# Kernel tuning notes

Hardware: AMD Instinct MI355X
Metric: run time of the kernel (lower is better)

## Reference

```python
import jax, jax.numpy as jnp
import numpy as np

D = 128   # opt.geometric_latent_dim
H = 132   # FCBlock hidden width (hardcoded in source)
B = 65536
K = 8

def setup_inputs() -> dict:
    key = jax.random.key(0)
    ks = jax.random.split(key, 16)
    s = lambda k, shp, fan: jax.random.normal(k, shp, jnp.float32) / np.sqrt(fan)
    return {
        "signal": jax.random.normal(ks[0], (B, D), jnp.float32),
        "components": jax.random.normal(ks[1], (K, B, D), jnp.float32),
        # message_map / update_map: Linear(D, D)
        "Wm": s(ks[2], (D, D), D), "bm": jnp.zeros((D,), jnp.float32),
        "Wu": s(ks[3], (D, D), D), "bu": jnp.zeros((D,), jnp.float32),
        "W0": s(ks[4], (H, 2 * D), 2 * D), "b0": jnp.zeros((H,), jnp.float32),
        "W1": s(ks[5], (H, H), H),         "b1": jnp.zeros((H,), jnp.float32),
        "W2": s(ks[6], (H, H), H),         "b2": jnp.zeros((H,), jnp.float32),
        "W3": s(ks[7], (D, H), H),         "b3": jnp.zeros((D,), jnp.float32),
    }

def reference(signal, components, Wm, bm, Wu, bu, W0, b0, W1, b1, W2, b2, W3, b3):
    # message_map applied to each component, then summed over components
    msgs = jnp.einsum('kbd,ed->kbe', components, Wm) + bm  # [K,B,D]
    right = msgs.sum(axis=0)                               # [B,D]
    # update_map
    right = right @ Wu.T + bu                              # [B,D]
    # joint_update: FCBlock on concat([signal, right])
    x = jnp.concatenate([signal, right], axis=-1)          # [B,2D]
    x = jax.nn.relu(x @ W0.T + b0)
    x = jax.nn.relu(x @ W1.T + b1)
    x = jax.nn.relu(x @ W2.T + b2)
    return x @ W3.T + b3                                   # [B,D]
```

## Files before the change

kernel.cpp:

```cpp
#include <hip/hip_runtime.h>
#include <stdint.h>

#define DD  128
#define HH  132
#define BB  65536
#define KKC 8
#define HP  144
#define KP  160

typedef short bf16x8 __attribute__((ext_vector_type(8)));
typedef float f32x4  __attribute__((ext_vector_type(4)));

__device__ __forceinline__ unsigned short f2b(float f){
  union{float f; unsigned u;} c; c.f = f;
  unsigned r = c.u + 0x7fffu + ((c.u >> 16) & 1u);
  return (unsigned short)(r >> 16);
}

__global__ void prepA(const float* __restrict__ Wm, const float* __restrict__ bm,
                      const float* __restrict__ Wu, const float* __restrict__ bu,
                      float* __restrict__ Wf, float* __restrict__ bfv){
  int idx = blockIdx.x * 256 + threadIdx.x;
  int i = idx >> 7, j = idx & 127;
  float acc = 0.f;
  for(int d = 0; d < DD; ++d)
    acc += Wu[i*DD + d] * Wm[d*DD + j];
  Wf[idx] = acc;
  if(j == 0){
    float a = 0.f;
    for(int d = 0; d < DD; ++d) a += Wu[i*DD + d] * bm[d];
    bfv[i] = (float)KKC * a + bu[i];
  }
}

__global__ void prepB(const float* __restrict__ W0, const float* __restrict__ b0,
                      const float* __restrict__ W1, const float* __restrict__ b1,
                      const float* __restrict__ W2, const float* __restrict__ b2,
                      const float* __restrict__ W3, const float* __restrict__ b3,
                      const float* __restrict__ Wf, const float* __restrict__ bfv,
                      unsigned short* __restrict__ w0s_p, unsigned short* __restrict__ w0rp,
                      unsigned short* __restrict__ w1p,  unsigned short* __restrict__ w2p,
                      unsigned short* __restrict__ w3p,
                      float* __restrict__ b0p, float* __restrict__ b1p,
                      float* __restrict__ b2p, float* __restrict__ b3p){
  int idx = blockIdx.x * 256 + threadIdx.x;
  if(idx < HP*DD){
    int n = idx >> 7, k = idx & 127;
    w0s_p[idx] = (n < HH) ? f2b(W0[n*(2*DD) + k]) : (unsigned short)0;
    return;
  }
  idx -= HP*DD;
  if(idx < HP*DD){
    int n = idx >> 7, k = idx & 127;
    float acc = 0.f;
    if(n < HH)
      for(int i = 0; i < DD; ++i)
        acc += W0[n*(2*DD) + DD + i] * Wf[i*DD + k];
    w0rp[idx] = (n < HH) ? f2b(acc) : (unsigned short)0;
    return;
  }
  idx -= HP*DD;
  if(idx < HP*KP){
    int n = idx / KP, k = idx % KP;
    w1p[idx] = (n < HH && k < HH) ? f2b(W1[n*HH + k]) : (unsigned short)0;
    return;
  }
  idx -= HP*KP;
  if(idx < HP*KP){
    int n = idx / KP, k = idx % KP;
    w2p[idx] = (n < HH && k < HH) ? f2b(W2[n*HH + k]) : (unsigned short)0;
    return;
  }
  idx -= HP*KP;
  if(idx < DD*KP){
    int n = idx / KP, k = idx % KP;
    w3p[idx] = (k < HH) ? f2b(W3[n*HH + k]) : (unsigned short)0;
    return;
  }
  idx -= DD*KP;
  if(idx < HP){
    float acc = 0.f;
    if(idx < HH){
      acc = b0[idx];
      for(int i = 0; i < DD; ++i) acc += W0[idx*(2*DD) + DD + i] * bfv[i];
    }
    b0p[idx] = acc;
    return;
  }
  idx -= HP;
  if(idx < HP){ b1p[idx] = (idx < HH) ? b1[idx] : 0.f; return; }
  idx -= HP;
  if(idx < HP){ b2p[idx] = (idx < HH) ? b2[idx] : 0.f; return; }
  idx -= HP;
  if(idx < DD){ b3p[idx] = b3[idx]; return; }
}

__global__ __launch_bounds__(256) void fused_msgprop(
    const float* __restrict__ signal,
    const float* __restrict__ comps,
    const unsigned short* __restrict__ w0s_p,
    const unsigned short* __restrict__ w0rp,
    const unsigned short* __restrict__ w1p,
    const unsigned short* __restrict__ w2p,
    const unsigned short* __restrict__ w3p,
    const float* __restrict__ b0p, const float* __restrict__ b1p,
    const float* __restrict__ b2p, const float* __restrict__ b3p,
    float* __restrict__ out)
{
  const int tid  = threadIdx.x;
  const int lane = tid & 63;
  const int wave = tid >> 6;
  const int m    = lane & 15;
  const int quad = lane >> 4;
  const int rowBase = blockIdx.x * 64 + wave * 16;

  __shared__ unsigned short lds[4][16][168];

  for(int t = tid; t < 4*16*16; t += 256){
    int wv = t >> 8, r = (t >> 4) & 15, c = t & 15;
    lds[wv][r][144 + c] = 0;
  }
  __syncthreads();

  const int arow = rowBase + m;

  bf16x8 sigf[4];
  {
    const float* srow = signal + (size_t)arow * DD;
    #pragma unroll
    for(int ki = 0; ki < 4; ++ki){
      f32x4 lo = *(const f32x4*)(srow + ki*32 + quad*8);
      f32x4 hi = *(const f32x4*)(srow + ki*32 + quad*8 + 4);
      bf16x8 p;
      #pragma unroll
      for(int j = 0; j < 4; ++j){ p[j] = (short)f2b(lo[j]); p[4+j] = (short)f2b(hi[j]); }
      sigf[ki] = p;
    }
  }

  bf16x8 compf[4];
  {
    float a[4][8];
    #pragma unroll
    for(int ki = 0; ki < 4; ++ki)
      #pragma unroll
      for(int j = 0; j < 8; ++j) a[ki][j] = 0.f;
    #pragma unroll
    for(int k = 0; k < KKC; ++k){
      const float* crow = comps + ((size_t)k * BB + arow) * DD;
      #pragma unroll
      for(int ki = 0; ki < 4; ++ki){
        f32x4 lo = *(const f32x4*)(crow + ki*32 + quad*8);
        f32x4 hi = *(const f32x4*)(crow + ki*32 + quad*8 + 4);
        #pragma unroll
        for(int j = 0; j < 4; ++j){ a[ki][j] += lo[j]; a[ki][4+j] += hi[j]; }
      }
    }
    #pragma unroll
    for(int ki = 0; ki < 4; ++ki){
      bf16x8 p;
      #pragma unroll
      for(int j = 0; j < 8; ++j) p[j] = (short)f2b(a[ki][j]);
      compf[ki] = p;
    }
  }

  #pragma unroll
  for(int nt = 0; nt < 9; ++nt){
    f32x4 acc = {0.f,0.f,0.f,0.f};
    const unsigned short* wr1 = w0s_p + (size_t)(nt*16 + m)*DD + quad*8;
    const unsigned short* wr2 = w0rp  + (size_t)(nt*16 + m)*DD + quad*8;
    #pragma unroll
    for(int ki = 0; ki < 4; ++ki){
      bf16x8 wf = *(const bf16x8*)(wr1 + ki*32);
      acc = __builtin_amdgcn_mfma_f32_16x16x32_bf16(sigf[ki], wf, acc, 0, 0, 0);
    }
    #pragma unroll
    for(int ki = 0; ki < 4; ++ki){
      bf16x8 wf = *(const bf16x8*)(wr2 + ki*32);
      acc = __builtin_amdgcn_mfma_f32_16x16x32_bf16(compf[ki], wf, acc, 0, 0, 0);
    }
    float bias = b0p[nt*16 + m];
    #pragma unroll
    for(int r = 0; r < 4; ++r){
      float v = acc[r] + bias;
      v = v > 0.f ? v : 0.f;
      lds[wave][quad*4 + r][nt*16 + m] = f2b(v);
    }
  }
  __syncthreads();

  bf16x8 hf[5];

  #pragma unroll
  for(int ki = 0; ki < 5; ++ki)
    hf[ki] = *(const bf16x8*)&lds[wave][m][ki*32 + quad*8];
  __syncthreads();
  #pragma unroll
  for(int nt = 0; nt < 9; ++nt){
    f32x4 acc = {0.f,0.f,0.f,0.f};
    const unsigned short* wr = w1p + (size_t)(nt*16 + m)*KP + quad*8;
    #pragma unroll
    for(int ki = 0; ki < 5; ++ki){
      bf16x8 wf = *(const bf16x8*)(wr + ki*32);
      acc = __builtin_amdgcn_mfma_f32_16x16x32_bf16(hf[ki], wf, acc, 0, 0, 0);
    }
    float bias = b1p[nt*16 + m];
    #pragma unroll
    for(int r = 0; r < 4; ++r){
      float v = acc[r] + bias;
      v = v > 0.f ? v : 0.f;
      lds[wave][quad*4 + r][nt*16 + m] = f2b(v);
    }
  }
  __syncthreads();

  #pragma unroll
  for(int ki = 0; ki < 5; ++ki)
    hf[ki] = *(const bf16x8*)&lds[wave][m][ki*32 + quad*8];
  __syncthreads();
  #pragma unroll
  for(int nt = 0; nt < 9; ++nt){
    f32x4 acc = {0.f,0.f,0.f,0.f};
    const unsigned short* wr = w2p + (size_t)(nt*16 + m)*KP + quad*8;
    #pragma unroll
    for(int ki = 0; ki < 5; ++ki){
      bf16x8 wf = *(const bf16x8*)(wr + ki*32);
      acc = __builtin_amdgcn_mfma_f32_16x16x32_bf16(hf[ki], wf, acc, 0, 0, 0);
    }
    float bias = b2p[nt*16 + m];
    #pragma unroll
    for(int r = 0; r < 4; ++r){
      float v = acc[r] + bias;
      v = v > 0.f ? v : 0.f;
      lds[wave][quad*4 + r][nt*16 + m] = f2b(v);
    }
  }
  __syncthreads();

  #pragma unroll
  for(int ki = 0; ki < 5; ++ki)
    hf[ki] = *(const bf16x8*)&lds[wave][m][ki*32 + quad*8];
  #pragma unroll
  for(int nt = 0; nt < 8; ++nt){
    f32x4 acc = {0.f,0.f,0.f,0.f};
    const unsigned short* wr = w3p + (size_t)(nt*16 + m)*KP + quad*8;
    #pragma unroll
    for(int ki = 0; ki < 5; ++ki){
      bf16x8 wf = *(const bf16x8*)(wr + ki*32);
      acc = __builtin_amdgcn_mfma_f32_16x16x32_bf16(hf[ki], wf, acc, 0, 0, 0);
    }
    float bias = b3p[nt*16 + m];
    #pragma unroll
    for(int r = 0; r < 4; ++r){
      int grow = rowBase + quad*4 + r;
      out[(size_t)grow*DD + nt*16 + m] = acc[r] + bias;
    }
  }
}

extern "C" void kernel_launch(void* const* d_in, const int* in_sizes, int n_in,
                              void* d_out, int out_size, void* d_ws, size_t ws_size,
                              hipStream_t stream){
  const float* signal = (const float*)d_in[0];
  const float* comps  = (const float*)d_in[1];
  const float* Wm = (const float*)d_in[2];
  const float* bm = (const float*)d_in[3];
  const float* Wu = (const float*)d_in[4];
  const float* bu = (const float*)d_in[5];
  const float* W0 = (const float*)d_in[6];
  const float* b0 = (const float*)d_in[7];
  const float* W1 = (const float*)d_in[8];
  const float* b1 = (const float*)d_in[9];
  const float* W2 = (const float*)d_in[10];
  const float* b2 = (const float*)d_in[11];
  const float* W3 = (const float*)d_in[12];
  const float* b3 = (const float*)d_in[13];

  char* ws = (char*)d_ws;
  float*          Wf    = (float*)(ws + 0);
  float*          bfv   = (float*)(ws + 65536);
  unsigned short* w0s_p = (unsigned short*)(ws + 66048);
  unsigned short* w0rp  = (unsigned short*)(ws + 102912);
  unsigned short* w1p   = (unsigned short*)(ws + 139776);
  unsigned short* w2p   = (unsigned short*)(ws + 185856);
  unsigned short* w3p   = (unsigned short*)(ws + 231936);
  float*          b0p   = (float*)(ws + 272896);
  float*          b1p   = (float*)(ws + 273472);
  float*          b2p   = (float*)(ws + 274048);
  float*          b3p   = (float*)(ws + 274624);

  hipLaunchKernelGGL(prepA, dim3(64), dim3(256), 0, stream, Wm, bm, Wu, bu, Wf, bfv);

  hipLaunchKernelGGL(prepB, dim3(407), dim3(256), 0, stream,
                     W0, b0, W1, b1, W2, b2, W3, b3, Wf, bfv,
                     w0s_p, w0rp, w1p, w2p, w3p, b0p, b1p, b2p, b3p);

  hipLaunchKernelGGL(fused_msgprop, dim3(BB/64), dim3(256), 0, stream,
                     signal, comps, w0s_p, w0rp, w1p, w2p, w3p,
                     b0p, b1p, b2p, b3p, (float*)d_out);
}
```

Before: 471.3 us.

## Split component summation into a streaming kernel and shrink MLP blocks to one wave

Moves the sum over the K=8 component tensors out of the fused MLP kernel into a separate, fully coalesced streaming kernel that writes a bf16 sum buffer. The MLP kernel now reads that compact buffer and runs as 64-thread single-wave blocks with a 16-row LDS tile. The goal is better bandwidth on the dominant 268MB component read, which the per-lane strided loads in the fused kernel used poorly. In exchange it adds a kernel launch plus a 16MB write and read round trip, and the many tiny blocks may hurt weight-load reuse.

```diff
diff --git a/kernel.cpp b/kernel.cpp
--- a/kernel.cpp
+++ b/kernel.cpp
@@ -9,6 +9,7 @@
 #define KP  160
 
 typedef short bf16x8 __attribute__((ext_vector_type(8)));
+typedef short bf16x4 __attribute__((ext_vector_type(4)));
 typedef float f32x4  __attribute__((ext_vector_type(4)));
 
 __device__ __forceinline__ unsigned short f2b(float f){
@@ -95,9 +96,24 @@
   if(idx < DD){ b3p[idx] = b3[idx]; return; }
 }
 
-__global__ __launch_bounds__(256) void fused_msgprop(
+__global__ __launch_bounds__(256, 8) void comp_sum(
+    const float* __restrict__ comps, unsigned short* __restrict__ sumb){
+  const size_t idx4 = ((size_t)blockIdx.x * 256 + threadIdx.x) * 4;
+  f32x4 a = {0.f,0.f,0.f,0.f};
+  #pragma unroll
+  for(int k = 0; k < KKC; ++k){
+    f32x4 v = *(const f32x4*)(comps + (size_t)k * BB * DD + idx4);
+    a += v;
+  }
+  bf16x4 p;
+  #pragma unroll
+  for(int j = 0; j < 4; ++j) p[j] = (short)f2b(a[j]);
+  *(bf16x4*)(sumb + idx4) = p;
+}
+
+__global__ __launch_bounds__(64, 4) void fused_mlp(
     const float* __restrict__ signal,
-    const float* __restrict__ comps,
+    const unsigned short* __restrict__ sumb,
     const unsigned short* __restrict__ w0s_p,
     const unsigned short* __restrict__ w0rp,
     const unsigned short* __restrict__ w1p,
@@ -108,21 +124,21 @@
     float* __restrict__ out)
 {
   const int tid  = threadIdx.x;
-  const int lane = tid & 63;
-  const int wave = tid >> 6;
-  const int m    = lane & 15;
-  const int quad = lane >> 4;
-  const int rowBase = blockIdx.x * 64 + wave * 16;
-
-  __shared__ unsigned short lds[4][16][168];
-
-  for(int t = tid; t < 4*16*16; t += 256){
-    int wv = t >> 8, r = (t >> 4) & 15, c = t & 15;
-    lds[wv][r][144 + c] = 0;
-  }
-  __syncthreads();
-
+  const int m    = tid & 15;
+  const int quad = tid >> 4;
+  const int rowBase = blockIdx.x * 16;
   const int arow = rowBase + m;
+
+  __shared__ unsigned short act[16][168];
+
+  for(int t = tid; t < 16*16; t += 64){
+    act[t >> 4][144 + (t & 15)] = 0;
+  }
+
+  bf16x8 sumf[4];
+  #pragma unroll
+  for(int ki = 0; ki < 4; ++ki)
+    sumf[ki] = *(const bf16x8*)(sumb + (size_t)arow*DD + ki*32 + quad*8);
 
   bf16x8 sigf[4];
   {
@@ -137,33 +153,7 @@
       sigf[ki] = p;
     }
   }
-
-  bf16x8 compf[4];
-  {
-    float a[4][8];
-    #pragma unroll
-    for(int ki = 0; ki < 4; ++ki)
-      #pragma unroll
-      for(int j = 0; j < 8; ++j) a[ki][j] = 0.f;
-    #pragma unroll
-    for(int k = 0; k < KKC; ++k){
-      const float* crow = comps + ((size_t)k * BB + arow) * DD;
-      #pragma unroll
-      for(int ki = 0; ki < 4; ++ki){
-        f32x4 lo = *(const f32x4*)(crow + ki*32 + quad*8);
-        f32x4 hi = *(const f32x4*)(crow + ki*32 + quad*8 + 4);
-        #pragma unroll
-        for(int j = 0; j < 4; ++j){ a[ki][j] += lo[j]; a[ki][4+j] += hi[j]; }
-      }
-    }
-    #pragma unroll
-    for(int ki = 0; ki < 4; ++ki){
-      bf16x8 p;
-      #pragma unroll
-      for(int j = 0; j < 8; ++j) p[j] = (short)f2b(a[ki][j]);
-      compf[ki] = p;
-    }
-  }
+  __syncthreads();
 
   #pragma unroll
   for(int nt = 0; nt < 9; ++nt){
@@ -178,14 +168,14 @@
     #pragma unroll
     for(int ki = 0; ki < 4; ++ki){
       bf16x8 wf = *(const bf16x8*)(wr2 + ki*32);
-      acc = __builtin_amdgcn_mfma_f32_16x16x32_bf16(compf[ki], wf, acc, 0, 0, 0);
+      acc = __builtin_amdgcn_mfma_f32_16x16x32_bf16(sumf[ki], wf, acc, 0, 0, 0);
     }
     float bias = b0p[nt*16 + m];
     #pragma unroll
     for(int r = 0; r < 4; ++r){
       float v = acc[r] + bias;
       v = v > 0.f ? v : 0.f;
-      lds[wave][quad*4 + r][nt*16 + m] = f2b(v);
+      act[quad*4 + r][nt*16 + m] = f2b(v);
     }
   }
   __syncthreads();
@@ -194,7 +184,7 @@
 
   #pragma unroll
   for(int ki = 0; ki < 5; ++ki)
-    hf[ki] = *(const bf16x8*)&lds[wave][m][ki*32 + quad*8];
+    hf[ki] = *(const bf16x8*)&act[m][ki*32 + quad*8];
   __syncthreads();
   #pragma unroll
   for(int nt = 0; nt < 9; ++nt){
@@ -210,14 +200,14 @@
     for(int r = 0; r < 4; ++r){
       float v = acc[r] + bias;
       v = v > 0.f ? v : 0.f;
-      lds[wave][quad*4 + r][nt*16 + m] = f2b(v);
+      act[quad*4 + r][nt*16 + m] = f2b(v);
     }
   }
   __syncthreads();
 
   #pragma unroll
   for(int ki = 0; ki < 5; ++ki)
-    hf[ki] = *(const bf16x8*)&lds[wave][m][ki*32 + quad*8];
+    hf[ki] = *(const bf16x8*)&act[m][ki*32 + quad*8];
   __syncthreads();
   #pragma unroll
   for(int nt = 0; nt < 9; ++nt){
@@ -233,14 +223,14 @@
     for(int r = 0; r < 4; ++r){
       float v = acc[r] + bias;
       v = v > 0.f ? v : 0.f;
-      lds[wave][quad*4 + r][nt*16 + m] = f2b(v);
+      act[quad*4 + r][nt*16 + m] = f2b(v);
     }
   }
   __syncthreads();
 
   #pragma unroll
   for(int ki = 0; ki < 5; ++ki)
-    hf[ki] = *(const bf16x8*)&lds[wave][m][ki*32 + quad*8];
+    hf[ki] = *(const bf16x8*)&act[m][ki*32 + quad*8];
   #pragma unroll
   for(int nt = 0; nt < 8; ++nt){
     f32x4 acc = {0.f,0.f,0.f,0.f};
@@ -289,6 +279,9 @@
   float*          b1p   = (float*)(ws + 273472);
   float*          b2p   = (float*)(ws + 274048);
   float*          b3p   = (float*)(ws + 274624);
+  unsigned short* sumb  = (unsigned short*)(ws + 275456);
+
+  hipLaunchKernelGGL(comp_sum, dim3(BB*DD/4/256), dim3(256), 0, stream, comps, sumb);
 
   hipLaunchKernelGGL(prepA, dim3(64), dim3(256), 0, stream, Wm, bm, Wu, bu, Wf, bfv);
 
@@ -296,7 +289,7 @@
                      W0, b0, W1, b1, W2, b2, W3, b3, Wf, bfv,
                      w0s_p, w0rp, w1p, w2p, w3p, b0p, b1p, b2p, b3p);
 
-  hipLaunchKernelGGL(fused_msgprop, dim3(BB/64), dim3(256), 0, stream,
-                     signal, comps, w0s_p, w0rp, w1p, w2p, w3p,
+  hipLaunchKernelGGL(fused_mlp, dim3(BB/16), dim3(64), 0, stream,
+                     signal, sumb, w0s_p, w0rp, w1p, w2p, w3p,
                      b0p, b1p, b2p, b3p, (float*)d_out);
 }
```

Measured after the change: 500.9 us. +6.3%, slower.
